# Kernel tuning notes

Measured on AMD Instinct MI355X. Metric: run time of the kernel, lower is better.

Reference implementation:

```python
import jax, jax.numpy as jnp
import numpy as np

B, C, D = 16, 128, 256


def setup_inputs() -> dict:
    key = jax.random.key(0)
    ks = jax.random.split(key, 12)
    s = 0.05
    return {
        "h_t": jax.random.normal(ks[0], (B, C, D), jnp.float32),
        "A_a": jax.random.normal(ks[1], (C, C), jnp.float32) * s,
        "A_m": jax.random.normal(ks[2], (C, C), jnp.float32) * s,
        "W1": jax.random.normal(ks[3], (2 * D, D), jnp.float32) * s,
        "b1": jax.random.normal(ks[4], (D,), jnp.float32) * s,
        "W2": jax.random.normal(ks[5], (D, 1), jnp.float32) * s,
        "b2": jax.random.normal(ks[6], (1,), jnp.float32) * s,
        "Wa": jax.random.normal(ks[7], (D, D), jnp.float32) * s,
        "ba": jax.random.normal(ks[8], (D,), jnp.float32) * s,
        "Wm": jax.random.normal(ks[9], (D, D), jnp.float32) * s,
        "bm": jax.random.normal(ks[10], (D,), jnp.float32) * s,
        "beta1": jnp.float32(1.0),
        "beta2": jnp.float32(1.0),
        "beta3": jnp.float32(1.0),
    }


def reference(h_t, A_a, A_m, W1, b1, W2, b2, Wa, ba, Wm, bm, beta1, beta2, beta3):
    d = h_t.shape[-1]
    # Pairwise edge-MLP score S[b,u,v] = sigmoid(W2 @ relu(W1 @ [h_u; h_v] + b1) + b2).
    # Split W1 into the half acting on h_u and the half acting on h_v, so the
    # (B,C,C,2D) concat never materializes (same math as Linear on the concat).
    pre_u = jnp.einsum('bud,dk->buk', h_t, W1[:d])        # (B,C,D)
    pre_v = jnp.einsum('bvd,dk->bvk', h_t, W1[d:])        # (B,C,D)
    hidden = jax.nn.relu(pre_u[:, :, None, :] + pre_v[:, None, :, :] + b1)  # (B,C,C,D)
    S = jax.nn.sigmoid(jnp.einsum('buvk,ko->buvo', hidden, W2)[..., 0] + b2[0])  # (B,C,C)

    # Additive aggregation: a_t[b,v,:] = sum_u (S*A_a)[b,u,v] * h_t[b,u,:]
    a_t = jnp.einsum('buv,bud->bvd', S * A_a, h_t)

    # Hadamard aggregation: m_t[b,v,d] = sum_u A_m[u,v] * h[b,u,d] * h[b,v,d]
    #                              = (A_m^T @ h_t) * h_t  (avoids (B,C,C,D) tensor)
    m_t = jnp.einsum('uv,bud->bvd', A_m, h_t) * h_t

    z_t = (beta1 * h_t
           + beta2 * (jnp.einsum('bvd,de->bve', a_t, Wa) + ba)
           + beta3 * (jnp.einsum('bvd,de->bve', m_t, Wm) + bm))
    return z_t
```

## Files before the change

### kernel.cpp

```cpp
#include <hip/hip_runtime.h>
#include <hip/hip_bf16.h>

#define B_ 16
#define C_ 128
#define D_ 256

typedef unsigned int uint32;
typedef unsigned short u16;
typedef __attribute__((ext_vector_type(8))) short s8v;
typedef __attribute__((ext_vector_type(4))) float f4v;

__device__ __forceinline__ u16 bfu(float x) {
  union { __hip_bfloat16 h; u16 s; } u;
  u.h = __float2bfloat16(x);
  return u.s;
}
__device__ __forceinline__ float2 bf2x(uint32 x) {
  return make_float2(__uint_as_float(x << 16), __uint_as_float(x & 0xffff0000u));
}

__global__ __launch_bounds__(256) void kprep(const float* __restrict__ h,
    const float* __restrict__ W1, const float* __restrict__ Wa,
    const float* __restrict__ Wm, const float* __restrict__ Am,
    const float* __restrict__ ba, const float* __restrict__ bm,
    const float* __restrict__ be2, const float* __restrict__ be3,
    u16* __restrict__ hb, u16* __restrict__ hbT, u16* __restrict__ w1t,
    u16* __restrict__ wcatT, u16* __restrict__ amT, float* __restrict__ bcat) {
  const int idx0 = blockIdx.x * 256 + threadIdx.x;
  const int stride = gridDim.x * 256;
  const float b2v = be2[0], b3v = be3[0];
  for (int i = idx0; i < B_ * C_ * D_; i += stride) hb[i] = bfu(h[i]);
  for (int i = idx0; i < B_ * C_ * D_; i += stride) {
    const int b = i >> 15, r = i & 32767, d = r >> 7, u = r & 127;
    hbT[i] = bfu(h[(b * C_ + u) * D_ + d]);
  }
  for (int i = idx0; i < 512 * 256; i += stride) {
    const int n = i >> 8, k = i & 255;
    const float v = (n < 256) ? W1[k * 256 + n] : W1[(256 + k) * 256 + (n - 256)];
    w1t[i] = bfu(v);
  }
  for (int i = idx0; i < 256 * 512; i += stride) {
    const int n = i >> 9, k = i & 511;
    const float v = (k < 256) ? b2v * Wa[k * 256 + n] : b3v * Wm[(k - 256) * 256 + n];
    wcatT[i] = bfu(v);
  }
  for (int i = idx0; i < C_ * C_; i += stride) {
    const int v = i >> 7, u = i & 127;
    amT[i] = bfu(Am[u * C_ + v]);
  }
  for (int i = idx0; i < D_; i += stride) bcat[i] = b2v * ba[i] + b3v * bm[i];
}

__global__ __launch_bounds__(256) void k1_mfma(const u16* __restrict__ hb,
    const u16* __restrict__ w1t, const float* __restrict__ b1,
    u16* __restrict__ P, u16* __restrict__ Q) {
  const int lane = threadIdx.x & 63;
  const int w = blockIdx.x * 4 + (threadIdx.x >> 6);
  const int nt = w & 31, mt = w >> 5;
  const int row0 = mt * 16, col0 = nt * 16;
  const int lr = lane & 15, lk = lane >> 4;
  const u16* ap = hb + (row0 + lr) * D_ + lk * 8;
  const u16* bp = w1t + (col0 + lr) * D_ + lk * 8;
  f4v acc = {0.f, 0.f, 0.f, 0.f};
#pragma unroll
  for (int ks = 0; ks < 8; ++ks) {
    const s8v af = *(const s8v*)(ap + ks * 32);
    const s8v bf = *(const s8v*)(bp + ks * 32);
    acc = __builtin_amdgcn_mfma_f32_16x16x32_bf16(af, bf, acc, 0, 0, 0);
  }
  const int col = col0 + lr;
  if (col0 < 256) {
#pragma unroll
    for (int r = 0; r < 4; ++r) {
      const int row = row0 + lk * 4 + r;
      P[row * D_ + col] = bfu(acc[r]);
    }
  } else {
    const float bb = b1[col - 256];
#pragma unroll
    for (int r = 0; r < 4; ++r) {
      const int row = row0 + lk * 4 + r;
      Q[row * D_ + (col - 256)] = bfu(acc[r] + bb);
    }
  }
}

__global__ __launch_bounds__(256) void k2_s(const u16* __restrict__ P,
    const u16* __restrict__ Q, const float* __restrict__ W2,
    const float* __restrict__ b2, const float* __restrict__ Aa,
    float* __restrict__ SA) {
  const int b = blockIdx.z;
  const int u0 = blockIdx.x * 16;
  const int v0 = blockIdx.y * 16;
  const int tid = threadIdx.x;
  __shared__ uint32 Pl[16][130];
  __shared__ uint32 Ql[16][130];
  const uint32* Pg = (const uint32*)(P + (b * C_ + u0) * D_);
  const uint32* Qg = (const uint32*)(Q + (b * C_ + v0) * D_);
#pragma unroll
  for (int i = 0; i < 8; ++i) {
    const int idx = i * 256 + tid;
    const int r = idx >> 7, kk = idx & 127;
    Pl[r][kk] = Pg[r * 128 + kk];
    Ql[r][kk] = Qg[r * 128 + kk];
  }
  __syncthreads();
  const int ul = tid & 15;
  const int vl = tid >> 4;
  const float4* __restrict__ w4 = (const float4*)W2;
  float a0 = 0.f, a1 = 0.f;
#pragma unroll 8
  for (int kk = 0; kk < 128; kk += 2) {
    const uint2 pu = *(const uint2*)&Pl[ul][kk];
    const uint2 qu = *(const uint2*)&Ql[vl][kk];
    const float4 wv = w4[kk >> 1];
    const float2 p0 = bf2x(pu.x), p1 = bf2x(pu.y);
    const float2 q0 = bf2x(qu.x), q1 = bf2x(qu.y);
    a0 = fmaf(fmaxf(p0.x + q0.x, 0.f), wv.x, a0);
    a0 = fmaf(fmaxf(p0.y + q0.y, 0.f), wv.y, a0);
    a1 = fmaf(fmaxf(p1.x + q1.x, 0.f), wv.z, a1);
    a1 = fmaf(fmaxf(p1.y + q1.y, 0.f), wv.w, a1);
  }
  const float s = 1.f / (1.f + __expf(-(a0 + a1 + b2[0])));
  const int u = u0 + ul, v = v0 + vl;
  SA[b * C_ * C_ + v * C_ + u] = s * Aa[u * C_ + v];
}

__global__ __launch_bounds__(256) void k3_mfma(const float* __restrict__ SA,
    const u16* __restrict__ amT, const u16* __restrict__ hbT,
    const float* __restrict__ h, u16* __restrict__ atcat) {
  const int lane = threadIdx.x & 63;
  const int w = blockIdx.x * 4 + (threadIdx.x >> 6);
  const int bt = w >> 7, rem = w & 127;
  const int mt = rem >> 4, nt = rem & 15;
  const int v0 = mt * 16, d0 = nt * 16;
  const int lr = lane & 15, lk = lane >> 4;
  const float* sap = SA + (bt * C_ + v0 + lr) * C_ + lk * 8;
  const u16* a2p = amT + (v0 + lr) * C_ + lk * 8;
  const u16* bp = hbT + (bt * D_ + d0 + lr) * C_ + lk * 8;
  f4v acca = {0.f, 0.f, 0.f, 0.f}, accm = {0.f, 0.f, 0.f, 0.f};
#pragma unroll
  for (int ks = 0; ks < 4; ++ks) {
    const float4 f0 = *(const float4*)(sap + ks * 32);
    const float4 f1 = *(const float4*)(sap + ks * 32 + 4);
    union { s8v v; u16 u[8]; } a1;
    a1.u[0] = bfu(f0.x); a1.u[1] = bfu(f0.y); a1.u[2] = bfu(f0.z); a1.u[3] = bfu(f0.w);
    a1.u[4] = bfu(f1.x); a1.u[5] = bfu(f1.y); a1.u[6] = bfu(f1.z); a1.u[7] = bfu(f1.w);
    const s8v a2 = *(const s8v*)(a2p + ks * 32);
    const s8v bf = *(const s8v*)(bp + ks * 32);
    acca = __builtin_amdgcn_mfma_f32_16x16x32_bf16(a1.v, bf, acca, 0, 0, 0);
    accm = __builtin_amdgcn_mfma_f32_16x16x32_bf16(a2, bf, accm, 0, 0, 0);
  }
  const int d = d0 + lr;
#pragma unroll
  for (int r = 0; r < 4; ++r) {
    const int vrow = v0 + lk * 4 + r;
    const int grow = bt * C_ + vrow;
    atcat[grow * 512 + d] = bfu(acca[r]);
    const float hv = h[grow * D_ + d];
    atcat[grow * 512 + 256 + d] = bfu(accm[r] * hv);
  }
}

__global__ __launch_bounds__(256) void k4_mfma(const u16* __restrict__ atcat,
    const u16* __restrict__ wcatT, const float* __restrict__ bcat,
    const float* __restrict__ h, const float* __restrict__ be1,
    float* __restrict__ z) {
  const int lane = threadIdx.x & 63;
  const int w = blockIdx.x * 4 + (threadIdx.x >> 6);
  const int nt = w & 15, mt = w >> 4;
  const int row0 = mt * 16, col0 = nt * 16;
  const int lr = lane & 15, lk = lane >> 4;
  const u16* ap = atcat + (row0 + lr) * 512 + lk * 8;
  const u16* bp = wcatT + (col0 + lr) * 512 + lk * 8;
  f4v acc = {0.f, 0.f, 0.f, 0.f};
#pragma unroll
  for (int ks = 0; ks < 16; ++ks) {
    const s8v af = *(const s8v*)(ap + ks * 32);
    const s8v bf = *(const s8v*)(bp + ks * 32);
    acc = __builtin_amdgcn_mfma_f32_16x16x32_bf16(af, bf, acc, 0, 0, 0);
  }
  const float b1v = be1[0];
  const int col = col0 + lr;
  const float bc = bcat[col];
#pragma unroll
  for (int r = 0; r < 4; ++r) {
    const int row = row0 + lk * 4 + r;
    z[row * D_ + col] = acc[r] + b1v * h[row * D_ + col] + bc;
  }
}

extern "C" void kernel_launch(void* const* d_in, const int* in_sizes, int n_in,
                              void* d_out, int out_size, void* d_ws, size_t ws_size,
                              hipStream_t stream) {
  const float* h   = (const float*)d_in[0];
  const float* Aa  = (const float*)d_in[1];
  const float* Am  = (const float*)d_in[2];
  const float* W1  = (const float*)d_in[3];
  const float* b1  = (const float*)d_in[4];
  const float* W2  = (const float*)d_in[5];
  const float* b2  = (const float*)d_in[6];
  const float* Wa  = (const float*)d_in[7];
  const float* ba  = (const float*)d_in[8];
  const float* Wm  = (const float*)d_in[9];
  const float* bm  = (const float*)d_in[10];
  const float* be1 = (const float*)d_in[11];
  const float* be2 = (const float*)d_in[12];
  const float* be3 = (const float*)d_in[13];
  float* z = (float*)d_out;

  char* wsb = (char*)d_ws;
  u16*   hb    = (u16*)(wsb);
  u16*   hbT   = (u16*)(wsb + (1 << 20));
  u16*   w1t   = (u16*)(wsb + (2 << 20));
  u16*   wcatT = (u16*)(wsb + (2 << 20) + (256 << 10));
  u16*   amT   = (u16*)(wsb + (2 << 20) + (512 << 10));
  float* bcat  = (float*)(wsb + (2 << 20) + (544 << 10));
  u16*   P     = (u16*)(wsb + (3 << 20));
  u16*   Q     = (u16*)(wsb + (4 << 20));
  float* SA    = (float*)(wsb + (5 << 20));
  u16*   atcat = (u16*)(wsb + (6 << 20));

  kprep  <<<1024, 256, 0, stream>>>(h, W1, Wa, Wm, Am, ba, bm, be2, be3,
                                    hb, hbT, w1t, wcatT, amT, bcat);
  k1_mfma<<<1024, 256, 0, stream>>>(hb, w1t, b1, P, Q);
  k2_s   <<<dim3(8, 8, 16), 256, 0, stream>>>(P, Q, W2, b2, Aa, SA);
  k3_mfma<<<512, 256, 0, stream>>>(SA, amT, hbT, h, atcat);
  k4_mfma<<<512, 256, 0, stream>>>(atcat, wcatT, bcat, h, be1, z);
}
```

Before: 123.3 us.

## Vectorize prep conversions, store SA as bf16, widen k2 shared loads

The grid-stride prep kernel becomes block-partitioned segments, each thread converting four elements with vector stores. The S*A_a matrix is written as bf16 instead of fp32, which halves its traffic and lets k3 load MFMA operands directly without converting. k2's global-to-shared copy uses 128-bit loads. Rounding SA to bf16 happens earlier, though k3 already converted it to bf16 before, so the numerics stay the same.

```diff
diff --git a/kernel.cpp b/kernel.cpp
--- a/kernel.cpp
+++ b/kernel.cpp
@@ -26,29 +26,66 @@
     const float* __restrict__ be2, const float* __restrict__ be3,
     u16* __restrict__ hb, u16* __restrict__ hbT, u16* __restrict__ w1t,
     u16* __restrict__ wcatT, u16* __restrict__ amT, float* __restrict__ bcat) {
-  const int idx0 = blockIdx.x * 256 + threadIdx.x;
-  const int stride = gridDim.x * 256;
-  const float b2v = be2[0], b3v = be3[0];
-  for (int i = idx0; i < B_ * C_ * D_; i += stride) hb[i] = bfu(h[i]);
-  for (int i = idx0; i < B_ * C_ * D_; i += stride) {
-    const int b = i >> 15, r = i & 32767, d = r >> 7, u = r & 127;
-    hbT[i] = bfu(h[(b * C_ + u) * D_ + d]);
-  }
-  for (int i = idx0; i < 512 * 256; i += stride) {
-    const int n = i >> 8, k = i & 255;
-    const float v = (n < 256) ? W1[k * 256 + n] : W1[(256 + k) * 256 + (n - 256)];
-    w1t[i] = bfu(v);
-  }
-  for (int i = idx0; i < 256 * 512; i += stride) {
-    const int n = i >> 9, k = i & 511;
-    const float v = (k < 256) ? b2v * Wa[k * 256 + n] : b3v * Wm[(k - 256) * 256 + n];
-    wcatT[i] = bfu(v);
-  }
-  for (int i = idx0; i < C_ * C_; i += stride) {
-    const int v = i >> 7, u = i & 127;
-    amT[i] = bfu(Am[u * C_ + v]);
-  }
-  for (int i = idx0; i < D_; i += stride) bcat[i] = b2v * ba[i] + b3v * bm[i];
+  const int blk = blockIdx.x;
+  const int tid = threadIdx.x;
+  if (blk < 512) {
+    const int i4 = (blk * 256 + tid) * 4;
+    const float4 v = *(const float4*)(h + i4);
+    ushort4 o; o.x = bfu(v.x); o.y = bfu(v.y); o.z = bfu(v.z); o.w = bfu(v.w);
+    *(ushort4*)(hb + i4) = o;
+  } else if (blk < 1024) {
+    const int i4 = ((blk - 512) * 256 + tid) * 4;
+    const int b = i4 >> 15;
+    const int r = i4 & 32767;
+    const int d = r >> 7, u0 = r & 127;
+    const float x0 = h[(b * C_ + u0 + 0) * D_ + d];
+    const float x1 = h[(b * C_ + u0 + 1) * D_ + d];
+    const float x2 = h[(b * C_ + u0 + 2) * D_ + d];
+    const float x3 = h[(b * C_ + u0 + 3) * D_ + d];
+    ushort4 o; o.x = bfu(x0); o.y = bfu(x1); o.z = bfu(x2); o.w = bfu(x3);
+    *(ushort4*)(hbT + i4) = o;
+  } else if (blk < 1152) {
+    const int i4 = ((blk - 1024) * 256 + tid) * 4;
+    const int n = i4 >> 8, k0 = i4 & 255;
+    float x0, x1, x2, x3;
+    if (n < 256) {
+      x0 = W1[(k0 + 0) * 256 + n]; x1 = W1[(k0 + 1) * 256 + n];
+      x2 = W1[(k0 + 2) * 256 + n]; x3 = W1[(k0 + 3) * 256 + n];
+    } else {
+      const int nn = n - 256;
+      x0 = W1[(256 + k0 + 0) * 256 + nn]; x1 = W1[(256 + k0 + 1) * 256 + nn];
+      x2 = W1[(256 + k0 + 2) * 256 + nn]; x3 = W1[(256 + k0 + 3) * 256 + nn];
+    }
+    ushort4 o; o.x = bfu(x0); o.y = bfu(x1); o.z = bfu(x2); o.w = bfu(x3);
+    *(ushort4*)(w1t + i4) = o;
+  } else if (blk < 1280) {
+    const float b2v = be2[0], b3v = be3[0];
+    const int i4 = ((blk - 1152) * 256 + tid) * 4;
+    const int n = i4 >> 9, k0 = i4 & 511;
+    float x0, x1, x2, x3;
+    if (k0 < 256) {
+      x0 = b2v * Wa[(k0 + 0) * 256 + n]; x1 = b2v * Wa[(k0 + 1) * 256 + n];
+      x2 = b2v * Wa[(k0 + 2) * 256 + n]; x3 = b2v * Wa[(k0 + 3) * 256 + n];
+    } else {
+      const int kk = k0 - 256;
+      x0 = b3v * Wm[(kk + 0) * 256 + n]; x1 = b3v * Wm[(kk + 1) * 256 + n];
+      x2 = b3v * Wm[(kk + 2) * 256 + n]; x3 = b3v * Wm[(kk + 3) * 256 + n];
+    }
+    ushort4 o; o.x = bfu(x0); o.y = bfu(x1); o.z = bfu(x2); o.w = bfu(x3);
+    *(ushort4*)(wcatT + i4) = o;
+  } else if (blk < 1296) {
+    const int i4 = ((blk - 1280) * 256 + tid) * 4;
+    const int v = i4 >> 7, u0 = i4 & 127;
+    const float x0 = Am[(u0 + 0) * C_ + v];
+    const float x1 = Am[(u0 + 1) * C_ + v];
+    const float x2 = Am[(u0 + 2) * C_ + v];
+    const float x3 = Am[(u0 + 3) * C_ + v];
+    ushort4 o; o.x = bfu(x0); o.y = bfu(x1); o.z = bfu(x2); o.w = bfu(x3);
+    *(ushort4*)(amT + i4) = o;
+  } else {
+    const float b2v = be2[0], b3v = be3[0];
+    bcat[tid] = b2v * ba[tid] + b3v * bm[tid];
+  }
 }
 
 __global__ __launch_bounds__(256) void k1_mfma(const u16* __restrict__ hb,
@@ -71,24 +108,20 @@
   const int col = col0 + lr;
   if (col0 < 256) {
 #pragma unroll
-    for (int r = 0; r < 4; ++r) {
-      const int row = row0 + lk * 4 + r;
-      P[row * D_ + col] = bfu(acc[r]);
-    }
+    for (int r = 0; r < 4; ++r)
+      P[(row0 + lk * 4 + r) * D_ + col] = bfu(acc[r]);
   } else {
     const float bb = b1[col - 256];
 #pragma unroll
-    for (int r = 0; r < 4; ++r) {
-      const int row = row0 + lk * 4 + r;
-      Q[row * D_ + (col - 256)] = bfu(acc[r] + bb);
-    }
+    for (int r = 0; r < 4; ++r)
+      Q[(row0 + lk * 4 + r) * D_ + (col - 256)] = bfu(acc[r] + bb);
   }
 }
 
 __global__ __launch_bounds__(256) void k2_s(const u16* __restrict__ P,
     const u16* __restrict__ Q, const float* __restrict__ W2,
     const float* __restrict__ b2, const float* __restrict__ Aa,
-    float* __restrict__ SA) {
+    u16* __restrict__ SA) {
   const int b = blockIdx.z;
   const int u0 = blockIdx.x * 16;
   const int v0 = blockIdx.y * 16;
@@ -97,12 +130,19 @@
   __shared__ uint32 Ql[16][130];
   const uint32* Pg = (const uint32*)(P + (b * C_ + u0) * D_);
   const uint32* Qg = (const uint32*)(Q + (b * C_ + v0) * D_);
-#pragma unroll
-  for (int i = 0; i < 8; ++i) {
-    const int idx = i * 256 + tid;
-    const int r = idx >> 7, kk = idx & 127;
-    Pl[r][kk] = Pg[r * 128 + kk];
-    Ql[r][kk] = Qg[r * 128 + kk];
+  {
+    const int r = tid >> 5;
+    const int c4 = (tid & 31) * 4;
+#pragma unroll
+    for (int half = 0; half < 2; ++half) {
+      const int rr = r + half * 8;
+      const uint4 pv = *(const uint4*)&Pg[rr * 128 + c4];
+      const uint4 qv = *(const uint4*)&Qg[rr * 128 + c4];
+      *(uint2*)&Pl[rr][c4]     = make_uint2(pv.x, pv.y);
+      *(uint2*)&Pl[rr][c4 + 2] = make_uint2(pv.z, pv.w);
+      *(uint2*)&Ql[rr][c4]     = make_uint2(qv.x, qv.y);
+      *(uint2*)&Ql[rr][c4 + 2] = make_uint2(qv.z, qv.w);
+    }
   }
   __syncthreads();
   const int ul = tid & 15;
@@ -123,10 +163,10 @@
   }
   const float s = 1.f / (1.f + __expf(-(a0 + a1 + b2[0])));
   const int u = u0 + ul, v = v0 + vl;
-  SA[b * C_ * C_ + v * C_ + u] = s * Aa[u * C_ + v];
-}
-
-__global__ __launch_bounds__(256) void k3_mfma(const float* __restrict__ SA,
+  SA[b * C_ * C_ + v * C_ + u] = bfu(s * Aa[u * C_ + v]);
+}
+
+__global__ __launch_bounds__(256) void k3_mfma(const u16* __restrict__ SA,
     const u16* __restrict__ amT, const u16* __restrict__ hbT,
     const float* __restrict__ h, u16* __restrict__ atcat) {
   const int lane = threadIdx.x & 63;
@@ -135,27 +175,22 @@
   const int mt = rem >> 4, nt = rem & 15;
   const int v0 = mt * 16, d0 = nt * 16;
   const int lr = lane & 15, lk = lane >> 4;
-  const float* sap = SA + (bt * C_ + v0 + lr) * C_ + lk * 8;
+  const u16* sap = SA + (bt * C_ + v0 + lr) * C_ + lk * 8;
   const u16* a2p = amT + (v0 + lr) * C_ + lk * 8;
   const u16* bp = hbT + (bt * D_ + d0 + lr) * C_ + lk * 8;
   f4v acca = {0.f, 0.f, 0.f, 0.f}, accm = {0.f, 0.f, 0.f, 0.f};
 #pragma unroll
   for (int ks = 0; ks < 4; ++ks) {
-    const float4 f0 = *(const float4*)(sap + ks * 32);
-    const float4 f1 = *(const float4*)(sap + ks * 32 + 4);
-    union { s8v v; u16 u[8]; } a1;
-    a1.u[0] = bfu(f0.x); a1.u[1] = bfu(f0.y); a1.u[2] = bfu(f0.z); a1.u[3] = bfu(f0.w);
-    a1.u[4] = bfu(f1.x); a1.u[5] = bfu(f1.y); a1.u[6] = bfu(f1.z); a1.u[7] = bfu(f1.w);
+    const s8v a1 = *(const s8v*)(sap + ks * 32);
     const s8v a2 = *(const s8v*)(a2p + ks * 32);
     const s8v bf = *(const s8v*)(bp + ks * 32);
-    acca = __builtin_amdgcn_mfma_f32_16x16x32_bf16(a1.v, bf, acca, 0, 0, 0);
+    acca = __builtin_amdgcn_mfma_f32_16x16x32_bf16(a1, bf, acca, 0, 0, 0);
     accm = __builtin_amdgcn_mfma_f32_16x16x32_bf16(a2, bf, accm, 0, 0, 0);
   }
   const int d = d0 + lr;
 #pragma unroll
   for (int r = 0; r < 4; ++r) {
-    const int vrow = v0 + lk * 4 + r;
-    const int grow = bt * C_ + vrow;
+    const int grow = bt * C_ + v0 + lk * 4 + r;
     atcat[grow * 512 + d] = bfu(acca[r]);
     const float hv = h[grow * D_ + d];
     atcat[grow * 512 + 256 + d] = bfu(accm[r] * hv);
@@ -218,10 +253,10 @@
   float* bcat  = (float*)(wsb + (2 << 20) + (544 << 10));
   u16*   P     = (u16*)(wsb + (3 << 20));
   u16*   Q     = (u16*)(wsb + (4 << 20));
-  float* SA    = (float*)(wsb + (5 << 20));
+  u16*   SA    = (u16*)(wsb + (5 << 20));
   u16*   atcat = (u16*)(wsb + (6 << 20));
 
-  kprep  <<<1024, 256, 0, stream>>>(h, W1, Wa, Wm, Am, ba, bm, be2, be3,
+  kprep  <<<1297, 256, 0, stream>>>(h, W1, Wa, Wm, Am, ba, bm, be2, be3,
                                     hb, hbT, w1t, wcatT, amT, bcat);
   k1_mfma<<<1024, 256, 0, stream>>>(hb, w1t, b1, P, Q);
   k2_s   <<<dim3(8, 8, 16), 256, 0, stream>>>(P, Q, W2, b2, Aa, SA);
```

Result: no change. 121.2 us (-1.7%).
